# Kernel tuning notes

Measured on AMD Instinct MI355X. Metric: run time of the kernel, lower is better.

The kernel has to match this reference:

```python
import jax, jax.numpy as jnp
import numpy as np


def setup_inputs() -> dict:
    key = jax.random.key(0)
    k1, k2, k3, k4, k5 = jax.random.split(key, 5)
    B, S, ENC, DEC = 32, 2048, 1024, 512
    hidden = jax.random.normal(k1, (B, DEC), dtype=jnp.float32)
    encoder_outputs = jax.random.normal(k2, (B, S, ENC), dtype=jnp.float32)
    W = jax.random.normal(k3, (DEC, ENC + DEC), dtype=jnp.float32) * (1.0 / np.sqrt(ENC + DEC))
    b = jax.random.normal(k4, (DEC,), dtype=jnp.float32) * 0.01
    v = jax.random.uniform(k5, (DEC,), dtype=jnp.float32)  # torch.rand init
    return {"hidden": hidden, "encoder_outputs": encoder_outputs, "W": W, "b": b, "v": v}


def reference(hidden, encoder_outputs, W, b, v):
    # hidden: [B, D_dec], encoder_outputs: [B, S, D_enc]
    # Concat order in original: (hidden, encoder_outputs) -> split W accordingly.
    D_dec = hidden.shape[-1]
    Wh = W[:, :D_dec]   # [D_dec, D_dec] acts on hidden
    We = W[:, D_dec:]   # [D_dec, D_enc] acts on encoder_outputs
    # energy: tanh(Linear(cat(hidden_repeated, enc))) == tanh(h@Wh^T + enc@We^T + b)
    h_proj = jnp.einsum('bd,ed->be', hidden, Wh)                 # [B, D_dec]
    e_proj = jnp.einsum('bse,de->bsd', encoder_outputs, We)      # [B, S, D_dec]
    energy = jnp.tanh(e_proj + h_proj[:, None, :] + b)           # [B, S, D_dec]
    # scores: v . energy per (b, s); softmax over src_len
    scores = jnp.einsum('d,bsd->bs', v, energy)                  # [B, S]
    attn = jax.nn.softmax(scores, axis=-1)
    return attn[:, None, :]                                       # [B, 1, S]
```

## Files before the change

### kernel.cpp

```cpp
#include <hip/hip_runtime.h>
#include <hip/hip_bf16.h>


typedef __attribute__((ext_vector_type(8))) short bf16x8;
typedef __attribute__((ext_vector_type(4))) float f32x4;

__device__ __forceinline__ ushort f2bf(float x) {
    __hip_bfloat16 h = __float2bfloat16(x);
    return *reinterpret_cast<ushort*>(&h);
}

__device__ __forceinline__ bf16x8 pack8(float4 a, float4 b) {
    bf16x8 o;
    o[0] = (short)f2bf(a.x); o[1] = (short)f2bf(a.y);
    o[2] = (short)f2bf(a.z); o[3] = (short)f2bf(a.w);
    o[4] = (short)f2bf(b.x); o[5] = (short)f2bf(b.y);
    o[6] = (short)f2bf(b.z); o[7] = (short)f2bf(b.w);
    return o;
}

#define WS_WBF   0
#define WS_HB    (1u << 20)
#define WS_SCORE ((1u << 20) + (64u << 10))

__global__ void prep_kernel(const float* __restrict__ W,
                            const float* __restrict__ hidden,
                            const float* __restrict__ bias,
                            ushort* __restrict__ Wbf,
                            float* __restrict__ hb,
                            float* __restrict__ score) {
    const int bid = blockIdx.x, tid = threadIdx.x;
    if (bid < 512) {
        int idx = bid * 256 + tid;
        int d  = idx >> 8;
        int e4 = (idx & 255) * 4;
        float4 f = *(const float4*)(W + (size_t)d * 1536 + 512 + e4);
        ushort4 u;
        u.x = f2bf(f.x); u.y = f2bf(f.y); u.z = f2bf(f.z); u.w = f2bf(f.w);
        *(ushort4*)(Wbf + (size_t)d * 1024 + e4) = u;
    } else if (bid < 576) {
        int idx = (bid - 512) * 256 + tid;
        int b = idx >> 9, d = idx & 511;
        const float4* hp = (const float4*)(hidden + b * 512);
        const float4* wp = (const float4*)(W + (size_t)d * 1536);
        float acc = 0.f;
#pragma unroll 8
        for (int j = 0; j < 128; ++j) {
            float4 h = hp[j], w = wp[j];
            acc += h.x * w.x + h.y * w.y + h.z * w.z + h.w * w.w;
        }
        hb[idx] = acc + bias[d];
    } else {
        int idx = (bid - 576) * 256 + tid;
        float4 z = {0.f, 0.f, 0.f, 0.f};
        *(float4*)(score + (size_t)idx * 4) = z;
    }
}

__launch_bounds__(256, 2)
__global__ void eproj_scores(const float* __restrict__ enc,
                             const ushort* __restrict__ Wbf,
                             const float* __restrict__ hb,
                             const float* __restrict__ v,
                             float* __restrict__ scores) {
    __shared__ alignas(16) float Abuf[2][4][2048];

    const int tid  = threadIdx.x;
    const int lane = tid & 63, w = tid >> 6;
    const int q = lane >> 4, ln = lane & 15;
    const int  nblk = blockIdx.x & 1;
    const long m0   = (long)(blockIdx.x >> 1) * 64;
    const int  bidx = (int)(m0 >> 11);
    const int  n0   = nblk * 256 + w * 64;

    f32x4 acc[4][4];
#pragma unroll
    for (int mt = 0; mt < 4; ++mt)
#pragma unroll
        for (int nt = 0; nt < 4; ++nt)
            acc[mt][nt] = (f32x4){0.f, 0.f, 0.f, 0.f};

    const ushort* bptr[4];
#pragma unroll
    for (int nt = 0; nt < 4; ++nt)
        bptr[nt] = Wbf + (size_t)(n0 + nt * 16 + ln) * 1024 + q * 8;

    int sA0[4], sA1[4];
#pragma unroll
    for (int mt = 0; mt < 4; ++mt) {
        int rA = mt * 16 + ln;
        sA0[mt] = (rA * 8 + ((2 * q)     ^ (rA & 7))) * 4;
        sA1[mt] = (rA * 8 + ((2 * q + 1) ^ (rA & 7))) * 4;
    }

    auto dma_group = [&](int h, int k0) {
#pragma unroll
        for (int st = 0; st < 4; ++st)
#pragma unroll
            for (int i = 0; i < 2; ++i) {
                int s = i * 256 + tid;
                int r = s >> 3;
                int c = (s & 7) ^ (r & 7);
                const float* g = enc + (m0 + r) * 1024 + k0 + st * 32 + c * 4;
                float* lb = &Abuf[h][st][(i * 256 + w * 64) * 4];
                __builtin_amdgcn_global_load_lds(
                    (const __attribute__((address_space(1))) void*)g,
                    (__attribute__((address_space(3))) void*)lb, 16, 0, 0);
            }
    };

    dma_group(0, 0);
    bf16x8 bfr[2][4];
#pragma unroll
    for (int nt = 0; nt < 4; ++nt)
        bfr[0][nt] = *(const bf16x8*)(bptr[nt]);

    for (int g = 0; g < 8; ++g) {
        __syncthreads();
        if (g < 7) dma_group((g + 1) & 1, (g + 1) * 128);

        const float* H = &Abuf[g & 1][0][0];
#pragma unroll
        for (int j = 0; j < 4; ++j) {
            const int kt = g * 4 + j;
            if (kt < 31) {
#pragma unroll
                for (int nt = 0; nt < 4; ++nt)
                    bfr[(j + 1) & 1][nt] =
                        *(const bf16x8*)(bptr[nt] + (size_t)(kt + 1) * 32);
            }
            const float* Ab = H + j * 2048;
#pragma unroll
            for (int mt = 0; mt < 4; ++mt) {
                float4 a0 = *(const float4*)(Ab + sA0[mt]);
                float4 a1 = *(const float4*)(Ab + sA1[mt]);
                bf16x8 af = pack8(a0, a1);
#pragma unroll
                for (int nt = 0; nt < 4; ++nt)
                    acc[mt][nt] = __builtin_amdgcn_mfma_f32_16x16x32_bf16(
                        af, bfr[j & 1][nt], acc[mt][nt], 0, 0, 0);
            }
        }
    }

    float partial[4][4];
#pragma unroll
    for (int mt = 0; mt < 4; ++mt)
#pragma unroll
        for (int r = 0; r < 4; ++r) partial[mt][r] = 0.f;

#pragma unroll
    for (int nt = 0; nt < 4; ++nt) {
        int d = n0 + nt * 16 + ln;
        float hbv = hb[bidx * 512 + d];
        float vv  = v[d];
#pragma unroll
        for (int mt = 0; mt < 4; ++mt)
#pragma unroll
            for (int r = 0; r < 4; ++r) {
                float x = acc[mt][nt][r] + hbv;
                float e = __expf(2.f * x);
                partial[mt][r] += vv * (1.f - 2.f / (e + 1.f));
            }
    }
#pragma unroll
    for (int mt = 0; mt < 4; ++mt)
#pragma unroll
        for (int r = 0; r < 4; ++r) {
            float s = partial[mt][r];
            s += __shfl_xor(s, 1);
            s += __shfl_xor(s, 2);
            s += __shfl_xor(s, 4);
            s += __shfl_xor(s, 8);
            partial[mt][r] = s;
        }

    __syncthreads();
    float* spart = (float*)Abuf;
    if (ln == 0) {
#pragma unroll
        for (int mt = 0; mt < 4; ++mt)
#pragma unroll
            for (int r = 0; r < 4; ++r)
                spart[w * 64 + mt * 16 + q * 4 + r] = partial[mt][r];
    }
    __syncthreads();
    if (tid < 64)
        atomicAdd(&scores[m0 + tid],
                  spart[tid] + spart[64 + tid] + spart[128 + tid] + spart[192 + tid]);
}

__global__ void softmax_kernel(const float* __restrict__ scores, float* __restrict__ out) {
    int b = blockIdx.x;
    const float* sc = scores + b * 2048;
    __shared__ float wred[4], wsum[4];

    float lmax = -1e30f;
    for (int i = threadIdx.x; i < 2048; i += 256) lmax = fmaxf(lmax, sc[i]);
#pragma unroll
    for (int m = 1; m < 64; m <<= 1) lmax = fmaxf(lmax, __shfl_xor(lmax, m));
    if ((threadIdx.x & 63) == 0) wred[threadIdx.x >> 6] = lmax;
    __syncthreads();
    float gmax = fmaxf(fmaxf(wred[0], wred[1]), fmaxf(wred[2], wred[3]));

    float lsum = 0.f;
    for (int i = threadIdx.x; i < 2048; i += 256) lsum += __expf(sc[i] - gmax);
#pragma unroll
    for (int m = 1; m < 64; m <<= 1) lsum += __shfl_xor(lsum, m);
    if ((threadIdx.x & 63) == 0) wsum[threadIdx.x >> 6] = lsum;
    __syncthreads();
    float inv = 1.f / (wsum[0] + wsum[1] + wsum[2] + wsum[3]);

    for (int i = threadIdx.x; i < 2048; i += 256)
        out[b * 2048 + i] = __expf(sc[i] - gmax) * inv;
}

extern "C" void kernel_launch(void* const* d_in, const int* in_sizes, int n_in,
                              void* d_out, int out_size, void* d_ws, size_t ws_size,
                              hipStream_t stream) {
    const float* hidden = (const float*)d_in[0];
    const float* enc    = (const float*)d_in[1];
    const float* W      = (const float*)d_in[2];
    const float* bias   = (const float*)d_in[3];
    const float* v      = (const float*)d_in[4];
    float* out = (float*)d_out;

    char* ws = (char*)d_ws;
    ushort* Wbf   = (ushort*)(ws + WS_WBF);
    float*  hb    = (float*)(ws + WS_HB);
    float*  score = (float*)(ws + WS_SCORE);

    hipLaunchKernelGGL(prep_kernel,  dim3(640),  dim3(256), 0, stream,
                       W, hidden, bias, Wbf, hb, score);
    hipLaunchKernelGGL(eproj_scores, dim3(2048), dim3(256), 0, stream,
                       enc, Wbf, hb, v, score);
    hipLaunchKernelGGL(softmax_kernel, dim3(32), dim3(256), 0, stream, score, out);
}
```

Measured before the change: 490.4 us.

## Stage encoder tiles through registers as bf16 in LDS with swizzled block order

```diff
diff --git a/kernel.cpp b/kernel.cpp
--- a/kernel.cpp
+++ b/kernel.cpp
@@ -57,19 +57,20 @@
     }
 }
 
-__launch_bounds__(256, 2)
+__launch_bounds__(256, 3)
 __global__ void eproj_scores(const float* __restrict__ enc,
                              const ushort* __restrict__ Wbf,
                              const float* __restrict__ hb,
                              const float* __restrict__ v,
                              float* __restrict__ scores) {
-    __shared__ alignas(16) float Abuf[2][4][2048];
+    __shared__ alignas(16) ushort Abuf[4][2048];
 
     const int tid  = threadIdx.x;
     const int lane = tid & 63, w = tid >> 6;
     const int q = lane >> 4, ln = lane & 15;
-    const int  nblk = blockIdx.x & 1;
-    const long m0   = (long)(blockIdx.x >> 1) * 64;
+    const int  swz  = (blockIdx.x & 7) * 256 + (blockIdx.x >> 3);
+    const int  nblk = swz & 1;
+    const long m0   = (long)(swz >> 1) * 64;
     const int  bidx = (int)(m0 >> 11);
     const int  n0   = nblk * 256 + w * 64;
 
@@ -85,56 +86,56 @@
     for (int nt = 0; nt < 4; ++nt)
         bptr[nt] = Wbf + (size_t)(n0 + nt * 16 + ln) * 1024 + q * 8;
 
-    int sA0[4], sA1[4];
+    const int sr = tid >> 2, sq = tid & 3;
+    const float* aptr = enc + (m0 + sr) * 1024 + sq * 8;
+    const int awoff = sr * 32 + ((sq ^ (sr & 3)) << 3);
+
+    int rdoff[4];
 #pragma unroll
     for (int mt = 0; mt < 4; ++mt) {
         int rA = mt * 16 + ln;
-        sA0[mt] = (rA * 8 + ((2 * q)     ^ (rA & 7))) * 4;
-        sA1[mt] = (rA * 8 + ((2 * q + 1) ^ (rA & 7))) * 4;
-    }
-
-    auto dma_group = [&](int h, int k0) {
-#pragma unroll
-        for (int st = 0; st < 4; ++st)
-#pragma unroll
-            for (int i = 0; i < 2; ++i) {
-                int s = i * 256 + tid;
-                int r = s >> 3;
-                int c = (s & 7) ^ (r & 7);
-                const float* g = enc + (m0 + r) * 1024 + k0 + st * 32 + c * 4;
-                float* lb = &Abuf[h][st][(i * 256 + w * 64) * 4];
-                __builtin_amdgcn_global_load_lds(
-                    (const __attribute__((address_space(1))) void*)g,
-                    (__attribute__((address_space(3))) void*)lb, 16, 0, 0);
-            }
-    };
-
-    dma_group(0, 0);
+        rdoff[mt] = rA * 32 + ((q ^ (rA & 3)) << 3);
+    }
+
+    float4 ar[2][2];
+    ar[0][0] = *(const float4*)(aptr);
+    ar[0][1] = *(const float4*)(aptr + 4);
+    ar[1][0] = *(const float4*)(aptr + 32);
+    ar[1][1] = *(const float4*)(aptr + 36);
+
     bf16x8 bfr[2][4];
 #pragma unroll
     for (int nt = 0; nt < 4; ++nt)
         bfr[0][nt] = *(const bf16x8*)(bptr[nt]);
 
+    *(bf16x8*)(&Abuf[0][awoff]) = pack8(ar[0][0], ar[0][1]);
+    ar[0][0] = *(const float4*)(aptr + 64);
+    ar[0][1] = *(const float4*)(aptr + 68);
+
     for (int g = 0; g < 8; ++g) {
-        __syncthreads();
-        if (g < 7) dma_group((g + 1) & 1, (g + 1) * 128);
-
-        const float* H = &Abuf[g & 1][0][0];
 #pragma unroll
         for (int j = 0; j < 4; ++j) {
             const int kt = g * 4 + j;
-            if (kt < 31) {
+            const int p  = (j + 1) & 1;
+            if (kt + 1 < 32) {
+                *(bf16x8*)(&Abuf[(j + 1) & 3][awoff]) = pack8(ar[p][0], ar[p][1]);
+                if (kt + 3 < 32) {
+                    ar[p][0] = *(const float4*)(aptr + (kt + 3) * 32);
+                    ar[p][1] = *(const float4*)(aptr + (kt + 3) * 32 + 4);
+                }
+                asm volatile("s_waitcnt lgkmcnt(0)" ::: "memory");
+            }
+            __builtin_amdgcn_s_barrier();
+            asm volatile("" ::: "memory");
+
+            if (kt + 1 < 32) {
 #pragma unroll
                 for (int nt = 0; nt < 4; ++nt)
-                    bfr[(j + 1) & 1][nt] =
-                        *(const bf16x8*)(bptr[nt] + (size_t)(kt + 1) * 32);
-            }
-            const float* Ab = H + j * 2048;
+                    bfr[p][nt] = *(const bf16x8*)(bptr[nt] + (size_t)(kt + 1) * 32);
+            }
 #pragma unroll
             for (int mt = 0; mt < 4; ++mt) {
-                float4 a0 = *(const float4*)(Ab + sA0[mt]);
-                float4 a1 = *(const float4*)(Ab + sA1[mt]);
-                bf16x8 af = pack8(a0, a1);
+                bf16x8 af = *(const bf16x8*)(&Abuf[j][rdoff[mt]]);
 #pragma unroll
                 for (int nt = 0; nt < 4; ++nt)
                     acc[mt][nt] = __builtin_amdgcn_mfma_f32_16x16x32_bf16(
```

Result: slower. 513.7 us (+4.7%).
